# Optimization experiments

Hardware: AMD Instinct MI355X
Metric: run time of the kernel (lower is better)

## Reference

```python
import jax, jax.numpy as jnp
import numpy as np

B, T, D = 8, 2048, 128


def setup_inputs() -> dict:
    key = jax.random.key(0)
    kq, kk, kv = jax.random.split(key, 3)
    q = jax.random.normal(kq, (B, T, D), dtype=jnp.float32)
    k = jax.random.normal(kk, (B, T, D), dtype=jnp.float32)
    v = jax.random.normal(kv, (B, T, D), dtype=jnp.float32)
    # causal mask, broadcast over batch; 0 -> masked
    mask = jnp.tril(jnp.ones((T, T), dtype=jnp.int32))[None, :, :]
    mode = jnp.float32(0.5)  # learnable scalar parameter (init 0.5)
    return {"q": q, "k": k, "v": v, "mask": mask, "mode": mode}


def reference(q, k, v, mask, mode):
    scale = D ** (-0.5)
    # meson score: -(Q K^T) * scale
    meson = -jnp.einsum("btd,bsd->bts", q, k) * scale
    # baryon score: Q against K with feature dim rolled by 1
    k_perm = jnp.roll(k, shift=1, axis=-1)
    baryon = jnp.einsum("btd,bsd->bts", q, k_perm) * scale
    alpha = jax.nn.sigmoid(mode)
    attn = alpha * meson + (1.0 - alpha) * baryon
    attn = jnp.where(mask == 0, -jnp.inf, attn)
    attn = jax.nn.softmax(attn, axis=-1)
    return jnp.einsum("bts,bsd->btd", attn, v)
```

## Files before the change

kernel.cpp:

```cpp
#include <hip/hip_runtime.h>
#include <hip/hip_bf16.h>
#include <cstdint>
#include <cstddef>


typedef __attribute__((ext_vector_type(8))) short short8;
typedef __attribute__((ext_vector_type(4))) float f32x4;

#define T_DIM 2048
#define D_DIM 128
#define B_DIM 8
#define SEGT 8
#define POSLOTS_PER_B 224
#define MLSLOTS_PER_B 288
#define LOG2E 1.4426950408889634f

__device__ __forceinline__ unsigned short f2bf(float f) {
  unsigned u = __builtin_bit_cast(unsigned, f);
  u += 0x7FFFu + ((u >> 16) & 1u);
  return (unsigned short)(u >> 16);
}
__device__ __forceinline__ float bf2f(unsigned short u) {
  return __uint_as_float(((unsigned)u) << 16);
}
__device__ __forceinline__ void gload_lds16(const void* g, void* l) {
  __builtin_amdgcn_global_load_lds(
      (const __attribute__((address_space(1))) unsigned int*)g,
      (__attribute__((address_space(3))) unsigned int*)l, 16, 0, 0);
}

__global__ __launch_bounds__(256) void prep_all(
    const float* __restrict__ q, const float* __restrict__ k, const float* __restrict__ v,
    const float* __restrict__ modep,
    unsigned short* __restrict__ qbf, unsigned short* __restrict__ kbf,
    unsigned short* __restrict__ vt)
{
  __shared__ unsigned short tile[64 * 136];
  const int b = blockIdx.x, s0 = blockIdx.y * 64;
  const int tid = threadIdx.x;
  const float alpha = 1.f / (1.f + __expf(-modep[0]));
  const float scale = 0.08838834764831845f;
  const float ca = -alpha * scale * LOG2E, cb = (1.f - alpha) * scale * LOG2E;

#pragma unroll
  for (int u = 0; u < 4; ++u) {
    int c = u * 256 + tid;
    int r = c >> 4, c8 = c & 15;
    size_t row = (size_t)b * T_DIM + s0 + r;
    float4 ka = *(const float4*)(k + row * D_DIM + c8 * 8);
    float4 kb2 = *(const float4*)(k + row * D_DIM + c8 * 8 + 4);
    short8 ko = { (short)f2bf(ka.x), (short)f2bf(ka.y), (short)f2bf(ka.z), (short)f2bf(ka.w),
                  (short)f2bf(kb2.x), (short)f2bf(kb2.y), (short)f2bf(kb2.z), (short)f2bf(kb2.w) };
    *(short8*)(kbf + row * D_DIM + c8 * 8) = ko;
    const float* qr = q + row * D_DIM;
    float e[9];
    float4 f0 = *(const float4*)(qr + c8 * 8);
    float4 f1 = *(const float4*)(qr + c8 * 8 + 4);
    e[0] = f0.x; e[1] = f0.y; e[2] = f0.z; e[3] = f0.w;
    e[4] = f1.x; e[5] = f1.y; e[6] = f1.z; e[7] = f1.w;
    e[8] = qr[(c8 * 8 + 8) & 127];
    short8 qo;
#pragma unroll
    for (int j = 0; j < 8; ++j) qo[j] = (short)f2bf(ca * e[j] + cb * e[j + 1]);
    *(short8*)(qbf + row * D_DIM + c8 * 8) = qo;
    float4 va = *(const float4*)(v + row * D_DIM + c8 * 8);
    float4 vb2 = *(const float4*)(v + row * D_DIM + c8 * 8 + 4);
    short8 vo = { (short)f2bf(va.x), (short)f2bf(va.y), (short)f2bf(va.z), (short)f2bf(va.w),
                  (short)f2bf(vb2.x), (short)f2bf(vb2.y), (short)f2bf(vb2.z), (short)f2bf(vb2.w) };
    *(short8*)(tile + r * 136 + c8 * 8) = vo;
  }
  __syncthreads();
#pragma unroll
  for (int u = 0; u < 8; ++u) {
    int c = u * 256 + tid;
    int d = c >> 4, sq = c & 15;
    ushort4 o = { tile[(sq * 4 + 0) * 136 + d], tile[(sq * 4 + 1) * 136 + d],
                  tile[(sq * 4 + 2) * 136 + d], tile[(sq * 4 + 3) * 136 + d] };
    *(ushort4*)(vt + ((size_t)b * D_DIM + d) * T_DIM + s0 + sq * 4) = o;
  }
}

__global__ __launch_bounds__(128, 4) void attn_kernel(
    const unsigned short* __restrict__ qbf, const unsigned short* __restrict__ kbf,
    const unsigned short* __restrict__ vt, float* __restrict__ out,
    unsigned short* __restrict__ po, float* __restrict__ ml)
{
  __shared__ uint4 smem4[1152];
  char* smem = (char*)smem4;
  const int tid = threadIdx.x;
  const int w = tid >> 6, lane = tid & 63;
  const int t16 = lane & 15, g = lane >> 4;
  const int b = blockIdx.x;
  const int c = 63 - (int)blockIdx.y;
  const int s = blockIdx.z;
  const int nt = c + 1;
  const int nseg = (nt + SEGT - 1) >> 3;
  if (s >= nseg) return;
  const int t0 = s * SEGT;
  const int t1 = min(nt, t0 + SEGT);
  const int qb16 = c * 32 + w * 16;

  char* kb = smem;
  char* vb = smem + 8192;
  char* pw = smem + 16384 + w * 1024;
  const unsigned short* kbase = kbf + (size_t)b * T_DIM * D_DIM;
  const unsigned short* vbase = vt + (size_t)b * D_DIM * T_DIM;

  short8 qf[4];
  {
    const unsigned short* qr = qbf + ((size_t)b * T_DIM + qb16 + t16) * D_DIM + g * 8;
#pragma unroll
    for (int dd = 0; dd < 4; ++dd) qf[dd] = *(const short8*)(qr + dd * 32);
  }

  f32x4 acc[8];
#pragma unroll
  for (int dt = 0; dt < 8; ++dt) acc[dt] = (f32x4){0.f, 0.f, 0.f, 0.f};
  float mrun[4] = {-1e30f, -1e30f, -1e30f, -1e30f};
  float lsum[4] = {0.f, 0.f, 0.f, 0.f};

  for (int kt = t0; kt < t1; ++kt) {
    const int kv0 = kt * 32;
    __syncthreads();
#pragma unroll
    for (int u = 0; u < 4; ++u) {
      int s_loc = w * 16 + u * 4 + (lane >> 4);
      int slot = (lane & 15) ^ (s_loc & 7);
      gload_lds16(kbase + (size_t)(kv0 + s_loc) * D_DIM + slot * 8,
                  kb + w * 4096 + u * 1024);
    }
#pragma unroll
    for (int u = 0; u < 4; ++u) {
      int d_loc = w * 64 + u * 16 + (lane >> 2);
      int vslot = (lane & 3) ^ (d_loc & 3);
      gload_lds16(vbase + (size_t)d_loc * T_DIM + kv0 + vslot * 8,
                  vb + w * 4096 + u * 1024);
    }
    __syncthreads();

    f32x4 sj[2];
#pragma unroll
    for (int jt = 0; jt < 2; ++jt) {
      int srow = jt * 16 + t16;
      int rb = srow * 256, swz = (srow & 7) << 4;
      f32x4 sc = (f32x4){0.f, 0.f, 0.f, 0.f};
#pragma unroll
      for (int dd = 0; dd < 4; ++dd) {
        short8 kf = *(const short8*)(kb + ((rb + dd * 64 + g * 16) ^ swz));
        sc = __builtin_amdgcn_mfma_f32_16x16x32_bf16(qf[dd], kf, sc, 0, 0, 0);
      }
      sj[jt] = sc;
    }

    if (kt == c) {
#pragma unroll
      for (int jt = 0; jt < 2; ++jt) {
        int sg = kv0 + jt * 16 + t16;
#pragma unroll
        for (int r = 0; r < 4; ++r) {
          int tg = qb16 + 4 * g + r;
          if (sg > tg) sj[jt][r] = -1e30f;
        }
      }
    }

    float lm[4];
    int ok = 1;
#pragma unroll
    for (int r = 0; r < 4; ++r) {
      lm[r] = fmaxf(sj[0][r], sj[1][r]);
      ok &= (lm[r] <= mrun[r] + 11.0f);
    }
    if (!__all(ok)) {
#pragma unroll
      for (int r = 0; r < 4; ++r) {
        float tm = lm[r];
        tm = fmaxf(tm, __shfl_xor(tm, 1));
        tm = fmaxf(tm, __shfl_xor(tm, 2));
        tm = fmaxf(tm, __shfl_xor(tm, 4));
        tm = fmaxf(tm, __shfl_xor(tm, 8));
        float mnew = fmaxf(mrun[r], tm);
        float corr = exp2f(mrun[r] - mnew);
        mrun[r] = mnew;
        lsum[r] *= corr;
#pragma unroll
        for (int dt = 0; dt < 8; ++dt) acc[dt][r] *= corr;
      }
    }

#pragma unroll
    for (int jt = 0; jt < 2; ++jt)
#pragma unroll
      for (int r = 0; r < 4; ++r) {
        float p = exp2f(sj[jt][r] - mrun[r]);
        lsum[r] += p;
        int row = 4 * g + r;
        *(unsigned short*)(pw + row * 64 + ((jt * 32 + t16 * 2) ^ ((row >> 2) << 4))) = f2bf(p);
      }

    short8 pf = *(const short8*)(pw + t16 * 64 + ((g * 16) ^ ((t16 >> 2) << 4)));
#pragma unroll
    for (int dt = 0; dt < 8; ++dt) {
      int d = dt * 16 + t16;
      short8 vf = *(const short8*)(vb + d * 64 + ((g * 16) ^ ((d & 3) << 4)));
      acc[dt] = __builtin_amdgcn_mfma_f32_16x16x32_bf16(pf, vf, acc[dt], 0, 0, 0);
    }
  }

  float lred[4];
#pragma unroll
  for (int r = 0; r < 4; ++r) {
    float v0 = lsum[r];
    v0 += __shfl_xor(v0, 1);
    v0 += __shfl_xor(v0, 2);
    v0 += __shfl_xor(v0, 4);
    v0 += __shfl_xor(v0, 8);
    lred[r] = v0;
  }

  if (nseg == 1) {
#pragma unroll
    for (int r = 0; r < 4; ++r) {
      float inv = 1.0f / lred[r];
#pragma unroll
      for (int dt = 0; dt < 8; ++dt)
        out[((size_t)b * T_DIM + qb16 + 4 * g + r) * D_DIM + dt * 16 + t16] = acc[dt][r] * inv;
    }
  } else {
    int pofs = 0;
    for (int cc = 0; cc < c; ++cc) pofs += ((cc + SEGT) >> 3) - 1;
    if (s == 0) {
#pragma unroll
      for (int r = 0; r < 4; ++r)
#pragma unroll
        for (int dt = 0; dt < 8; ++dt)
          out[((size_t)b * T_DIM + qb16 + 4 * g + r) * D_DIM + dt * 16 + t16] = acc[dt][r];
    } else {
      unsigned short* pob = po + ((size_t)b * POSLOTS_PER_B + pofs + (s - 1)) * 4096;
#pragma unroll
      for (int r = 0; r < 4; ++r) {
        int rb = w * 16 + 4 * g + r;
#pragma unroll
        for (int dt = 0; dt < 8; ++dt)
          pob[rb * 128 + dt * 16 + t16] = f2bf(acc[dt][r]);
      }
    }
    if (t16 == 0) {
      const size_t mlslot = (size_t)b * MLSLOTS_PER_B + pofs + c + s;
#pragma unroll
      for (int r = 0; r < 4; ++r) {
        int rb = w * 16 + 4 * g + r;
        ml[mlslot * 64 + rb] = mrun[r];
        ml[mlslot * 64 + 32 + rb] = lred[r];
      }
    }
  }
}

__global__ __launch_bounds__(256) void combine_kernel(
    const unsigned short* __restrict__ po, const float* __restrict__ ml,
    float* __restrict__ out)
{
  const int tid = threadIdx.x;
  const int b = blockIdx.x;
  const int c = SEGT + (int)blockIdx.y;
  const int nt = c + 1;
  const int nseg = (nt + SEGT - 1) >> 3;
  int pofs = 0;
  for (int cc = 0; cc < c; ++cc) pofs += ((cc + SEGT) >> 3) - 1;
  const size_t mlbase = (size_t)b * MLSLOTS_PER_B + pofs + c;
  const size_t pobase = (size_t)b * POSLOTS_PER_B + pofs;

  __shared__ float wgt[32][8];
  if (tid < 32) {
    float M = -1e30f;
    for (int s = 0; s < nseg; ++s)
      M = fmaxf(M, ml[(mlbase + s) * 64 + tid]);
    float L = 0.f;
    for (int s = 0; s < nseg; ++s) {
      float e = exp2f(ml[(mlbase + s) * 64 + tid] - M);
      wgt[tid][s] = e;
      L += e * ml[(mlbase + s) * 64 + 32 + tid];
    }
    float invL = 1.f / L;
    for (int s = 0; s < nseg; ++s) wgt[tid][s] *= invL;
  }
  __syncthreads();

#pragma unroll
  for (int it = 0; it < 2; ++it) {
    int vid = it * 256 + tid;
    int r = vid >> 4, ch = vid & 15;
    float* op = out + ((size_t)b * T_DIM + c * 32 + r) * D_DIM + ch * 8;
    float4 a0 = *(const float4*)op;
    float4 a1 = *(const float4*)(op + 4);
    float w0 = wgt[r][0];
    float o[8] = { w0 * a0.x, w0 * a0.y, w0 * a0.z, w0 * a0.w,
                   w0 * a1.x, w0 * a1.y, w0 * a1.z, w0 * a1.w };
    for (int s = 1; s < nseg; ++s) {
      short8 pv = *(const short8*)(po + (pobase + s - 1) * 4096 + r * 128 + ch * 8);
      float ws = wgt[r][s];
#pragma unroll
      for (int j = 0; j < 8; ++j) o[j] += ws * bf2f((unsigned short)pv[j]);
    }
    *(float4*)op = (float4){o[0], o[1], o[2], o[3]};
    *(float4*)(op + 4) = (float4){o[4], o[5], o[6], o[7]};
  }
}

extern "C" void kernel_launch(void* const* d_in, const int* in_sizes, int n_in,
                              void* d_out, int out_size, void* d_ws, size_t ws_size,
                              hipStream_t stream) {
  const float* q = (const float*)d_in[0];
  const float* k = (const float*)d_in[1];
  const float* v = (const float*)d_in[2];
  const float* mode = (const float*)d_in[4];
  float* out = (float*)d_out;

  char* ws = (char*)d_ws;
  unsigned short* qbf = (unsigned short*)(ws);
  unsigned short* kbf = (unsigned short*)(ws + 4194304);
  unsigned short* vtb = (unsigned short*)(ws + 8388608);
  unsigned short* po  = (unsigned short*)(ws + 12582912);
  float*          ml  = (float*)(ws + 27262976);

  prep_all<<<dim3(B_DIM, T_DIM / 64), 256, 0, stream>>>(q, k, v, mode, qbf, kbf, vtb);
  attn_kernel<<<dim3(B_DIM, 64, SEGT), 128, 0, stream>>>(qbf, kbf, vtb, out, po, ml);
  combine_kernel<<<dim3(B_DIM, 64 - SEGT), 256, 0, stream>>>(po, ml, out);
}
```

Before: 53.20 us.

## Fuse Q scaling into attention kernel and route all segment partials through workspace

```diff
diff --git a/kernel.cpp b/kernel.cpp
--- a/kernel.cpp
+++ b/kernel.cpp
@@ -11,7 +11,6 @@
 #define D_DIM 128
 #define B_DIM 8
 #define SEGT 8
-#define POSLOTS_PER_B 224
 #define MLSLOTS_PER_B 288
 #define LOG2E 1.4426950408889634f
 
@@ -29,19 +28,13 @@
       (__attribute__((address_space(3))) unsigned int*)l, 16, 0, 0);
 }
 
-__global__ __launch_bounds__(256) void prep_all(
-    const float* __restrict__ q, const float* __restrict__ k, const float* __restrict__ v,
-    const float* __restrict__ modep,
-    unsigned short* __restrict__ qbf, unsigned short* __restrict__ kbf,
-    unsigned short* __restrict__ vt)
+__global__ __launch_bounds__(256) void prep_kv(
+    const float* __restrict__ k, const float* __restrict__ v,
+    unsigned short* __restrict__ kbf, unsigned short* __restrict__ vt)
 {
   __shared__ unsigned short tile[64 * 136];
   const int b = blockIdx.x, s0 = blockIdx.y * 64;
   const int tid = threadIdx.x;
-  const float alpha = 1.f / (1.f + __expf(-modep[0]));
-  const float scale = 0.08838834764831845f;
-  const float ca = -alpha * scale * LOG2E, cb = (1.f - alpha) * scale * LOG2E;
-
 #pragma unroll
   for (int u = 0; u < 4; ++u) {
     int c = u * 256 + tid;
@@ -52,17 +45,6 @@
     short8 ko = { (short)f2bf(ka.x), (short)f2bf(ka.y), (short)f2bf(ka.z), (short)f2bf(ka.w),
                   (short)f2bf(kb2.x), (short)f2bf(kb2.y), (short)f2bf(kb2.z), (short)f2bf(kb2.w) };
     *(short8*)(kbf + row * D_DIM + c8 * 8) = ko;
-    const float* qr = q + row * D_DIM;
-    float e[9];
-    float4 f0 = *(const float4*)(qr + c8 * 8);
-    float4 f1 = *(const float4*)(qr + c8 * 8 + 4);
-    e[0] = f0.x; e[1] = f0.y; e[2] = f0.z; e[3] = f0.w;
-    e[4] = f1.x; e[5] = f1.y; e[6] = f1.z; e[7] = f1.w;
-    e[8] = qr[(c8 * 8 + 8) & 127];
-    short8 qo;
-#pragma unroll
-    for (int j = 0; j < 8; ++j) qo[j] = (short)f2bf(ca * e[j] + cb * e[j + 1]);
-    *(short8*)(qbf + row * D_DIM + c8 * 8) = qo;
     float4 va = *(const float4*)(v + row * D_DIM + c8 * 8);
     float4 vb2 = *(const float4*)(v + row * D_DIM + c8 * 8 + 4);
     short8 vo = { (short)f2bf(va.x), (short)f2bf(va.y), (short)f2bf(va.z), (short)f2bf(va.w),
@@ -81,9 +63,9 @@
 }
 
 __global__ __launch_bounds__(128, 4) void attn_kernel(
-    const unsigned short* __restrict__ qbf, const unsigned short* __restrict__ kbf,
-    const unsigned short* __restrict__ vt, float* __restrict__ out,
-    unsigned short* __restrict__ po, float* __restrict__ ml)
+    const float* __restrict__ q, const unsigned short* __restrict__ kbf,
+    const unsigned short* __restrict__ vt, const float* __restrict__ modep,
+    float* __restrict__ out, unsigned short* __restrict__ po, float* __restrict__ ml)
 {
   __shared__ uint4 smem4[1152];
   char* smem = (char*)smem4;
@@ -106,11 +88,26 @@
   const unsigned short* kbase = kbf + (size_t)b * T_DIM * D_DIM;
   const unsigned short* vbase = vt + (size_t)b * D_DIM * T_DIM;
 
+  const float alpha = 1.f / (1.f + __expf(-modep[0]));
+  const float scale = 0.08838834764831845f;
+  const float ca = -alpha * scale * LOG2E, cb = (1.f - alpha) * scale * LOG2E;
   short8 qf[4];
   {
-    const unsigned short* qr = qbf + ((size_t)b * T_DIM + qb16 + t16) * D_DIM + g * 8;
-#pragma unroll
-    for (int dd = 0; dd < 4; ++dd) qf[dd] = *(const short8*)(qr + dd * 32);
+    const float* qr = q + ((size_t)b * T_DIM + qb16 + t16) * D_DIM;
+#pragma unroll
+    for (int dd = 0; dd < 4; ++dd) {
+      int dstart = dd * 32 + g * 8;
+      float e[9];
+      float4 f0 = *(const float4*)(qr + dstart);
+      float4 f1 = *(const float4*)(qr + dstart + 4);
+      e[0] = f0.x; e[1] = f0.y; e[2] = f0.z; e[3] = f0.w;
+      e[4] = f1.x; e[5] = f1.y; e[6] = f1.z; e[7] = f1.w;
+      e[8] = qr[(dstart + 8) & 127];
+      short8 qv;
+#pragma unroll
+      for (int i = 0; i < 8; ++i) qv[i] = (short)f2bf(ca * e[i] + cb * e[i + 1]);
+      qf[dd] = qv;
+    }
   }
 
   f32x4 acc[8];
@@ -229,29 +226,21 @@
   } else {
     int pofs = 0;
     for (int cc = 0; cc < c; ++cc) pofs += ((cc + SEGT) >> 3) - 1;
-    if (s == 0) {
-#pragma unroll
-      for (int r = 0; r < 4; ++r)
-#pragma unroll
-        for (int dt = 0; dt < 8; ++dt)
-          out[((size_t)b * T_DIM + qb16 + 4 * g + r) * D_DIM + dt * 16 + t16] = acc[dt][r];
-    } else {
-      unsigned short* pob = po + ((size_t)b * POSLOTS_PER_B + pofs + (s - 1)) * 4096;
+    const size_t slot = (size_t)b * MLSLOTS_PER_B + pofs + c + s;
+    unsigned short* pob = po + slot * 4096;
+#pragma unroll
+    for (int r = 0; r < 4; ++r) {
+      int rb = w * 16 + 4 * g + r;
+#pragma unroll
+      for (int dt = 0; dt < 8; ++dt)
+        pob[rb * 128 + dt * 16 + t16] = f2bf(acc[dt][r]);
+    }
+    if (t16 == 0) {
 #pragma unroll
       for (int r = 0; r < 4; ++r) {
         int rb = w * 16 + 4 * g + r;
-#pragma unroll
-        for (int dt = 0; dt < 8; ++dt)
-          pob[rb * 128 + dt * 16 + t16] = f2bf(acc[dt][r]);
-      }
-    }
-    if (t16 == 0) {
-      const size_t mlslot = (size_t)b * MLSLOTS_PER_B + pofs + c + s;
-#pragma unroll
-      for (int r = 0; r < 4; ++r) {
-        int rb = w * 16 + 4 * g + r;
-        ml[mlslot * 64 + rb] = mrun[r];
-        ml[mlslot * 64 + 32 + rb] = lred[r];
+        ml[slot * 64 + rb] = mrun[r];
+        ml[slot * 64 + 32 + rb] = lred[r];
       }
     }
   }
@@ -268,19 +257,18 @@
   const int nseg = (nt + SEGT - 1) >> 3;
   int pofs = 0;
   for (int cc = 0; cc < c; ++cc) pofs += ((cc + SEGT) >> 3) - 1;
-  const size_t mlbase = (size_t)b * MLSLOTS_PER_B + pofs + c;
-  const size_t pobase = (size_t)b * POSLOTS_PER_B + pofs;
+  const size_t slot0 = (size_t)b * MLSLOTS_PER_B + pofs + c;
 
   __shared__ float wgt[32][8];
   if (tid < 32) {
     float M = -1e30f;
     for (int s = 0; s < nseg; ++s)
-      M = fmaxf(M, ml[(mlbase + s) * 64 + tid]);
+      M = fmaxf(M, ml[(slot0 + s) * 64 + tid]);
     float L = 0.f;
     for (int s = 0; s < nseg; ++s) {
-      float e = exp2f(ml[(mlbase + s) * 64 + tid] - M);
+      float e = exp2f(ml[(slot0 + s) * 64 + tid] - M);
       wgt[tid][s] = e;
-      L += e * ml[(mlbase + s) * 64 + 32 + tid];
+      L += e * ml[(slot0 + s) * 64 + 32 + tid];
     }
     float invL = 1.f / L;
     for (int s = 0; s < nseg; ++s) wgt[tid][s] *= invL;
@@ -291,18 +279,14 @@
   for (int it = 0; it < 2; ++it) {
     int vid = it * 256 + tid;
     int r = vid >> 4, ch = vid & 15;
+    float o[8] = {0.f, 0.f, 0.f, 0.f, 0.f, 0.f, 0.f, 0.f};
+    for (int s = 0; s < nseg; ++s) {
+      short8 pv = *(const short8*)(po + (slot0 + s) * 4096 + r * 128 + ch * 8);
+      float ws = wgt[r][s];
+#pragma unroll
+      for (int j = 0; j < 8; ++j) o[j] += ws * bf2f((unsigned short)pv[j]);
+    }
     float* op = out + ((size_t)b * T_DIM + c * 32 + r) * D_DIM + ch * 8;
-    float4 a0 = *(const float4*)op;
-    float4 a1 = *(const float4*)(op + 4);
-    float w0 = wgt[r][0];
-    float o[8] = { w0 * a0.x, w0 * a0.y, w0 * a0.z, w0 * a0.w,
-                   w0 * a1.x, w0 * a1.y, w0 * a1.z, w0 * a1.w };
-    for (int s = 1; s < nseg; ++s) {
-      short8 pv = *(const short8*)(po + (pobase + s - 1) * 4096 + r * 128 + ch * 8);
-      float ws = wgt[r][s];
-#pragma unroll
-      for (int j = 0; j < 8; ++j) o[j] += ws * bf2f((unsigned short)pv[j]);
-    }
     *(float4*)op = (float4){o[0], o[1], o[2], o[3]};
     *(float4*)(op + 4) = (float4){o[4], o[5], o[6], o[7]};
   }
@@ -318,13 +302,12 @@
   float* out = (float*)d_out;
 
   char* ws = (char*)d_ws;
-  unsigned short* qbf = (unsigned short*)(ws);
-  unsigned short* kbf = (unsigned short*)(ws + 4194304);
-  unsigned short* vtb = (unsigned short*)(ws + 8388608);
-  unsigned short* po  = (unsigned short*)(ws + 12582912);
+  unsigned short* kbf = (unsigned short*)(ws);
+  unsigned short* vtb = (unsigned short*)(ws + 4194304);
+  unsigned short* po  = (unsigned short*)(ws + 8388608);
   float*          ml  = (float*)(ws + 27262976);
 
-  prep_all<<<dim3(B_DIM, T_DIM / 64), 256, 0, stream>>>(q, k, v, mode, qbf, kbf, vtb);
-  attn_kernel<<<dim3(B_DIM, 64, SEGT), 128, 0, stream>>>(qbf, kbf, vtb, out, po, ml);
+  prep_kv<<<dim3(B_DIM, T_DIM / 64), 256, 0, stream>>>(k, v, kbf, vtb);
+  attn_kernel<<<dim3(B_DIM, 64, SEGT), 128, 0, stream>>>(q, kbf, vtb, mode, out, po, ml);
   combine_kernel<<<dim3(B_DIM, 64 - SEGT), 256, 0, stream>>>(po, ml, out);
 }
```

Measured after the change: 55.59 us. +4.5%, slower.

## Double-buffer K in LDS and prefetch V into registers across KV tiles

Applied to the files above, without the earlier changes.

```diff
diff --git a/kernel.cpp b/kernel.cpp
--- a/kernel.cpp
+++ b/kernel.cpp
@@ -11,7 +11,6 @@
 #define D_DIM 128
 #define B_DIM 8
 #define SEGT 8
-#define POSLOTS_PER_B 224
 #define MLSLOTS_PER_B 288
 #define LOG2E 1.4426950408889634f
 
@@ -100,8 +99,6 @@
   const int t1 = min(nt, t0 + SEGT);
   const int qb16 = c * 32 + w * 16;
 
-  char* kb = smem;
-  char* vb = smem + 8192;
   char* pw = smem + 16384 + w * 1024;
   const unsigned short* kbase = kbf + (size_t)b * T_DIM * D_DIM;
   const unsigned short* vbase = vt + (size_t)b * D_DIM * T_DIM;
@@ -119,9 +116,9 @@
   float mrun[4] = {-1e30f, -1e30f, -1e30f, -1e30f};
   float lsum[4] = {0.f, 0.f, 0.f, 0.f};
 
-  for (int kt = t0; kt < t1; ++kt) {
+  auto stageK = [&](int cur, int kt) {
     const int kv0 = kt * 32;
-    __syncthreads();
+    char* kb = smem + cur * 8192;
 #pragma unroll
     for (int u = 0; u < 4; ++u) {
       int s_loc = w * 16 + u * 4 + (lane >> 4);
@@ -129,14 +126,30 @@
       gload_lds16(kbase + (size_t)(kv0 + s_loc) * D_DIM + slot * 8,
                   kb + w * 4096 + u * 1024);
     }
-#pragma unroll
-    for (int u = 0; u < 4; ++u) {
-      int d_loc = w * 64 + u * 16 + (lane >> 2);
-      int vslot = (lane & 3) ^ (d_loc & 3);
-      gload_lds16(vbase + (size_t)d_loc * T_DIM + kv0 + vslot * 8,
-                  vb + w * 4096 + u * 1024);
-    }
-    __syncthreads();
+  };
+  auto vload = [&](short8* vbuf, int kt) {
+    const int kv0 = kt * 32;
+#pragma unroll
+    for (int dt = 0; dt < 8; ++dt)
+      vbuf[dt] = *(const short8*)(vbase + (size_t)(dt * 16 + t16) * T_DIM + kv0 + g * 8);
+  };
+
+  short8 vcur[8], vnext[8];
+  stageK(0, t0);
+  vload(vcur, t0);
+  asm volatile("s_waitcnt vmcnt(0)" ::: "memory");
+  __builtin_amdgcn_s_barrier();
+  __builtin_amdgcn_sched_barrier(0);
+  int cur = 0;
+
+  for (int kt = t0; kt < t1; ++kt) {
+    const int kv0 = kt * 32;
+    const bool more = (kt + 1 < t1);
+    if (more) {
+      stageK(cur ^ 1, kt + 1);
+      vload(vnext, kt + 1);
+    }
+    char* kb = smem + cur * 8192;
 
     f32x4 sj[2];
 #pragma unroll
@@ -200,11 +213,17 @@
 
     short8 pf = *(const short8*)(pw + t16 * 64 + ((g * 16) ^ ((t16 >> 2) << 4)));
 #pragma unroll
-    for (int dt = 0; dt < 8; ++dt) {
-      int d = dt * 16 + t16;
-      short8 vf = *(const short8*)(vb + d * 64 + ((g * 16) ^ ((d & 3) << 4)));
-      acc[dt] = __builtin_amdgcn_mfma_f32_16x16x32_bf16(pf, vf, acc[dt], 0, 0, 0);
-    }
+    for (int dt = 0; dt < 8; ++dt)
+      acc[dt] = __builtin_amdgcn_mfma_f32_16x16x32_bf16(pf, vcur[dt], acc[dt], 0, 0, 0);
+
+    if (more) {
+      asm volatile("s_waitcnt vmcnt(8)" ::: "memory");
+#pragma unroll
+      for (int dt = 0; dt < 8; ++dt) vcur[dt] = vnext[dt];
+    }
+    __builtin_amdgcn_s_barrier();
+    __builtin_amdgcn_sched_barrier(0);
+    cur ^= 1;
   }
 
   float lred[4];
@@ -229,29 +248,21 @@
   } else {
     int pofs = 0;
     for (int cc = 0; cc < c; ++cc) pofs += ((cc + SEGT) >> 3) - 1;
-    if (s == 0) {
-#pragma unroll
-      for (int r = 0; r < 4; ++r)
-#pragma unroll
-        for (int dt = 0; dt < 8; ++dt)
-          out[((size_t)b * T_DIM + qb16 + 4 * g + r) * D_DIM + dt * 16 + t16] = acc[dt][r];
-    } else {
-      unsigned short* pob = po + ((size_t)b * POSLOTS_PER_B + pofs + (s - 1)) * 4096;
+    const size_t slot = (size_t)b * MLSLOTS_PER_B + pofs + c + s;
+    unsigned short* pob = po + slot * 4096;
+#pragma unroll
+    for (int r = 0; r < 4; ++r) {
+      int rb = w * 16 + 4 * g + r;
+#pragma unroll
+      for (int dt = 0; dt < 8; ++dt)
+        pob[rb * 128 + dt * 16 + t16] = f2bf(acc[dt][r]);
+    }
+    if (t16 == 0) {
 #pragma unroll
       for (int r = 0; r < 4; ++r) {
         int rb = w * 16 + 4 * g + r;
-#pragma unroll
-        for (int dt = 0; dt < 8; ++dt)
-          pob[rb * 128 + dt * 16 + t16] = f2bf(acc[dt][r]);
-      }
-    }
-    if (t16 == 0) {
-      const size_t mlslot = (size_t)b * MLSLOTS_PER_B + pofs + c + s;
-#pragma unroll
-      for (int r = 0; r < 4; ++r) {
-        int rb = w * 16 + 4 * g + r;
-        ml[mlslot * 64 + rb] = mrun[r];
-        ml[mlslot * 64 + 32 + rb] = lred[r];
+        ml[slot * 64 + rb] = mrun[r];
+        ml[slot * 64 + 32 + rb] = lred[r];
       }
     }
   }
@@ -268,19 +279,18 @@
   const int nseg = (nt + SEGT - 1) >> 3;
   int pofs = 0;
   for (int cc = 0; cc < c; ++cc) pofs += ((cc + SEGT) >> 3) - 1;
-  const size_t mlbase = (size_t)b * MLSLOTS_PER_B + pofs + c;
-  const size_t pobase = (size_t)b * POSLOTS_PER_B + pofs;
+  const size_t slot0 = (size_t)b * MLSLOTS_PER_B + pofs + c;
 
   __shared__ float wgt[32][8];
   if (tid < 32) {
     float M = -1e30f;
     for (int s = 0; s < nseg; ++s)
-      M = fmaxf(M, ml[(mlbase + s) * 64 + tid]);
+      M = fmaxf(M, ml[(slot0 + s) * 64 + tid]);
     float L = 0.f;
     for (int s = 0; s < nseg; ++s) {
-      float e = exp2f(ml[(mlbase + s) * 64 + tid] - M);
+      float e = exp2f(ml[(slot0 + s) * 64 + tid] - M);
       wgt[tid][s] = e;
-      L += e * ml[(mlbase + s) * 64 + 32 + tid];
+      L += e * ml[(slot0 + s) * 64 + 32 + tid];
     }
     float invL = 1.f / L;
     for (int s = 0; s < nseg; ++s) wgt[tid][s] *= invL;
@@ -291,18 +301,14 @@
   for (int it = 0; it < 2; ++it) {
     int vid = it * 256 + tid;
     int r = vid >> 4, ch = vid & 15;
+    float o[8] = {0.f, 0.f, 0.f, 0.f, 0.f, 0.f, 0.f, 0.f};
+    for (int s = 0; s < nseg; ++s) {
+      short8 pv = *(const short8*)(po + (slot0 + s) * 4096 + r * 128 + ch * 8);
+      float ws = wgt[r][s];
+#pragma unroll
+      for (int j = 0; j < 8; ++j) o[j] += ws * bf2f((unsigned short)pv[j]);
+    }
     float* op = out + ((size_t)b * T_DIM + c * 32 + r) * D_DIM + ch * 8;
-    float4 a0 = *(const float4*)op;
-    float4 a1 = *(const float4*)(op + 4);
-    float w0 = wgt[r][0];
-    float o[8] = { w0 * a0.x, w0 * a0.y, w0 * a0.z, w0 * a0.w,
-                   w0 * a1.x, w0 * a1.y, w0 * a1.z, w0 * a1.w };
-    for (int s = 1; s < nseg; ++s) {
-      short8 pv = *(const short8*)(po + (pobase + s - 1) * 4096 + r * 128 + ch * 8);
-      float ws = wgt[r][s];
-#pragma unroll
-      for (int j = 0; j < 8; ++j) o[j] += ws * bf2f((unsigned short)pv[j]);
-    }
     *(float4*)op = (float4){o[0], o[1], o[2], o[3]};
     *(float4*)(op + 4) = (float4){o[4], o[5], o[6], o[7]};
   }
@@ -322,7 +328,7 @@
   unsigned short* kbf = (unsigned short*)(ws + 4194304);
   unsigned short* vtb = (unsigned short*)(ws + 8388608);
   unsigned short* po  = (unsigned short*)(ws + 12582912);
-  float*          ml  = (float*)(ws + 27262976);
+  float*          ml  = (float*)(ws + 31457280);
 
   prep_all<<<dim3(B_DIM, T_DIM / 64), 256, 0, stream>>>(q, k, v, mode, qbf, kbf, vtb);
   attn_kernel<<<dim3(B_DIM, 64, SEGT), 128, 0, stream>>>(qbf, kbf, vtb, out, po, ml);
```

Measured after the change: 143.7 us. +170.1%, slower.
